# Optimization experiments

Measured on AMD Instinct MI355X. Metric: run time of the kernel, lower is better.

Reference implementation:

```python
import jax, jax.numpy as jnp
import numpy as np

N = 100000
E = 1000000
N_FEAT = 128
N_HID = 16
N_HEAD = 8
HIDDEN = N_HID * N_HEAD  # 128
N_CLASS = 64
NEG_SLOPE = 0.2


def layer_norm(x, g, b, eps=1e-5):
    mu = x.mean(-1, keepdims=True)
    var = ((x - mu) ** 2).mean(-1, keepdims=True)
    return (x - mu) * jax.lax.rsqrt(var + eps) * g + b


def gat_conv(x, src, dst, W, a_src, a_dst, bias, concat):
    # Standard GATConv math (PyG): project, per-head additive attention,
    # softmax over incoming edges (self-loops included), weighted scatter-sum.
    H, C = a_src.shape
    n = x.shape[0]
    h = (x @ W).reshape(n, H, C)                      # [N,H,C]
    al = jnp.einsum('nhc,hc->nh', h, a_src)           # [N,H]
    ar = jnp.einsum('nhc,hc->nh', h, a_dst)
    e = jax.nn.leaky_relu(al[src] + ar[dst], NEG_SLOPE)  # [E',H]
    m = jax.ops.segment_max(e, dst, num_segments=n)
    m = jnp.where(jnp.isfinite(m), m, 0.0)
    ee = jnp.exp(e - m[dst])
    den = jax.ops.segment_sum(ee, dst, num_segments=n)
    alpha = ee / (den[dst] + 1e-16)                   # [E',H]
    out = jax.ops.segment_sum(h[src] * alpha[:, :, None], dst, num_segments=n)
    out = out.reshape(n, H * C) if concat else out.mean(1)
    return out + bias, h, alpha


def setup_inputs() -> dict:
    key = jax.random.key(0)
    ks = jax.random.split(key, 20)
    s = lambda *sh: 1.0 / np.sqrt(sh[-1])
    inp = {
        'x': jax.random.normal(ks[0], (N, N_FEAT), jnp.float32),
        'edge_index': jax.random.randint(ks[1], (2, E), 0, N, jnp.int32),
        # layer 1: n_feat -> n_hid x n_head (concat)
        'W1': jax.random.normal(ks[2], (N_FEAT, HIDDEN), jnp.float32) * s(N_FEAT),
        'a_src1': jax.random.normal(ks[3], (N_HEAD, N_HID), jnp.float32) * s(N_HID),
        'a_dst1': jax.random.normal(ks[4], (N_HEAD, N_HID), jnp.float32) * s(N_HID),
        'b1': jnp.zeros((HIDDEN,), jnp.float32),
        'g1': jnp.ones((HIDDEN,), jnp.float32),
        'be1': jnp.zeros((HIDDEN,), jnp.float32),
        # layer 2: hidden -> hidden (concat)
        'W2': jax.random.normal(ks[5], (HIDDEN, HIDDEN), jnp.float32) * s(HIDDEN),
        'a_src2': jax.random.normal(ks[6], (N_HEAD, N_HID), jnp.float32) * s(N_HID),
        'a_dst2': jax.random.normal(ks[7], (N_HEAD, N_HID), jnp.float32) * s(N_HID),
        'b2': jnp.zeros((HIDDEN,), jnp.float32),
        'g2': jnp.ones((HIDDEN,), jnp.float32),
        'be2': jnp.zeros((HIDDEN,), jnp.float32),
        # out layer: hidden -> n_class, 1 head, concat=False
        'W3': jax.random.normal(ks[8], (HIDDEN, N_CLASS), jnp.float32) * s(HIDDEN),
        'a_src3': jax.random.normal(ks[9], (1, N_CLASS), jnp.float32) * s(N_CLASS),
        'a_dst3': jax.random.normal(ks[10], (1, N_CLASS), jnp.float32) * s(N_CLASS),
        'b3': jnp.zeros((N_CLASS,), jnp.float32),
        'g3': jnp.ones((N_CLASS,), jnp.float32),
        'be3': jnp.zeros((N_CLASS,), jnp.float32),
    }
    return inp


def reference(x, edge_index, W1, a_src1, a_dst1, b1, g1, be1,
              W2, a_src2, a_dst2, b2, g2, be2,
              W3, a_src3, a_dst3, b3, g3, be3):
    # add self loops (GATConv default)
    loops = jnp.arange(N, dtype=edge_index.dtype)
    src = jnp.concatenate([edge_index[0], loops])
    dst = jnp.concatenate([edge_index[1], loops])
    # Transductive path, eval mode (dropout is identity)
    x, _, _ = gat_conv(x, src, dst, W1, a_src1, a_dst1, b1, concat=True)
    x = jax.nn.elu(layer_norm(x, g1, be1))
    x, _, _ = gat_conv(x, src, dst, W2, a_src2, a_dst2, b2, concat=True)
    x = jax.nn.elu(layer_norm(x, g2, be2))
    x, _, _ = gat_conv(x, src, dst, W3, a_src3, a_dst3, b3, concat=False)
    x = layer_norm(x, g3, be3)
    return x
```

## Files before the change

### kernel.cpp

```cpp
#include <hip/hip_runtime.h>
#include <math.h>

#define N_NODES 100000
#define N_EDGES 1000000
#define EP_EDGES (N_EDGES + N_NODES)
#define NBKT ((N_NODES + 255) / 256)
#define PAD 48
#define NB_COUNT ((EP_EDGES + 4095) / 4096)
#define NB_WT ((128 * 128 + 128 * 64 + 255) / 256)

typedef short bf16x8 __attribute__((ext_vector_type(8)));
typedef float f32x4 __attribute__((ext_vector_type(4)));


__device__ inline unsigned bf16pack(float a, float b) {
    unsigned ua = __float_as_uint(a);
    unsigned ub = __float_as_uint(b);
    ua += 0x7FFFu + ((ua >> 16) & 1u);
    ub += 0x7FFFu + ((ub >> 16) & 1u);
    return (ua >> 16) | (ub & 0xFFFF0000u);
}

__device__ inline unsigned short bf16r(float a) {
    unsigned u = __float_as_uint(a);
    u += 0x7FFFu + ((u >> 16) & 1u);
    return (unsigned short)(u >> 16);
}

__device__ inline float bf16f(unsigned short v) {
    return __uint_as_float(((unsigned)v) << 16);
}

__device__ inline int swz(int o) { return o ^ (((o >> 8) & 7) << 4); }


__global__ void prep_count(const int* __restrict__ ei, int* __restrict__ bktCnt,
                           const float* __restrict__ W1, const float* __restrict__ W2,
                           const float* __restrict__ W3, unsigned short* __restrict__ Wt1,
                           unsigned short* __restrict__ Wt2, unsigned short* __restrict__ Wt3) {
    __shared__ int hist[NBKT];
    int tid = threadIdx.x;
    int b = blockIdx.x;
    if (b < NB_COUNT) {
        for (int j = tid; j < NBKT; j += 256) hist[j] = 0;
        __syncthreads();
        int e0 = b * 4096;
        int e1 = min(e0 + 4096, EP_EDGES);
        for (int e = e0 + tid; e < e1; e += 256) {
            int d = (e < N_EDGES) ? ei[N_EDGES + e] : (e - N_EDGES);
            atomicAdd(&hist[d >> 8], 1);
        }
        __syncthreads();
        for (int j = tid; j < NBKT; j += 256) {
            int c = hist[j];
            if (c) atomicAdd(&bktCnt[j], c);
        }
    } else {
        int t = (b - NB_COUNT) * 256 + tid;
        if (t < 128 * 128) {
            int k = t >> 7, c = t & 127;
            Wt1[c * 128 + k] = bf16r(W1[t]);
            Wt2[c * 128 + k] = bf16r(W2[t]);
        }
        int t3 = t - 128 * 128;
        if (t3 >= 0 && t3 < 128 * 64) {
            int k = t3 >> 6, c = t3 & 63;
            Wt3[c * 128 + k] = bf16r(W3[t3]);
        }
    }
}

__global__ void bkt_scan(const int* __restrict__ bktCnt, int* __restrict__ bktBase,
                         int* __restrict__ bktCursor) {
    __shared__ int tmp[512];
    int tid = threadIdx.x;
    int v = (tid < NBKT) ? bktCnt[tid] : 0;
    tmp[tid] = v;
    __syncthreads();
    int run = v;
    for (int off = 1; off < 512; off <<= 1) {
        int add = (tid >= off) ? tmp[tid - off] : 0;
        __syncthreads();
        run += add;
        tmp[tid] = run;
        __syncthreads();
    }
    if (tid <= NBKT) {
        int base = run - v;
        bktBase[tid] = base;
        if (tid < NBKT) bktCursor[tid] = base;
    }
}

__global__ void bkt_scatter(const int* __restrict__ ei, int* __restrict__ bktCursor,
                            unsigned* __restrict__ bktEdges) {
    __shared__ int hist[NBKT], chunk[NBKT];
    int tid = threadIdx.x;
    for (int j = tid; j < NBKT; j += 256) hist[j] = 0;
    __syncthreads();
    int e0 = blockIdx.x * 2048;
    int e1 = min(e0 + 2048, EP_EDGES);
    for (int e = e0 + tid; e < e1; e += 256) {
        int d = (e < N_EDGES) ? ei[N_EDGES + e] : (e - N_EDGES);
        atomicAdd(&hist[d >> 8], 1);
    }
    __syncthreads();
    for (int j = tid; j < NBKT; j += 256) {
        int c = hist[j];
        chunk[j] = c ? atomicAdd(&bktCursor[j], c) : 0;
        hist[j] = 0;
    }
    __syncthreads();
    for (int e = e0 + tid; e < e1; e += 256) {
        int s, d;
        if (e < N_EDGES) { s = ei[e]; d = ei[N_EDGES + e]; }
        else             { s = d = e - N_EDGES; }
        int b = d >> 8;
        int off = atomicAdd(&hist[b], 1);
        bktEdges[chunk[b] + off] = (unsigned)s | ((unsigned)(d & 255) << 24);
    }
}

__global__ void bkt_final(const unsigned* __restrict__ bktEdges, const int* __restrict__ bktBase,
                          int* __restrict__ deg_arr, int* __restrict__ pad_src) {
    __shared__ int hist[256], cur[256];
    int tid = threadIdx.x;
    int b = blockIdx.x;
    int base = bktBase[b], end = bktBase[b + 1];
    hist[tid] = 0;
    cur[tid] = 0;
    __syncthreads();
    for (int i = base + tid; i < end; i += 256)
        atomicAdd(&hist[bktEdges[i] >> 24], 1);
    __syncthreads();
    int node = b * 256 + tid;
    if (node < N_NODES) deg_arr[node] = min(hist[tid], PAD);
    __syncthreads();
    for (int i = base + tid; i < end; i += 256) {
        unsigned u = bktEdges[i];
        int d = u >> 24;
        int pos = atomicAdd(&cur[d], 1);
        if (pos < PAD)
            pad_src[(size_t)(b * 256 + d) * PAD + pos] = (int)(u & 0xFFFFFFu);
    }
    __syncthreads();
    for (int idx = tid; idx < 256 * PAD; idx += 256) {
        int dloc = idx / PAD, j = idx % PAD;
        int nd = b * 256 + dloc;
        if (nd < N_NODES) {
            int dg = min(hist[dloc], PAD);
            int lim = min(PAD, max(16, dg + 7));
            if (j >= dg && j < lim)
                pad_src[(size_t)nd * PAD + j] = nd;
        }
    }
}


template <int COUT, int H, bool IN_F32>
__launch_bounds__(256)
__global__ void gemm_mfma(const void* __restrict__ Xv, const unsigned short* __restrict__ Wt,
                          const float* __restrict__ a_src, const float* __restrict__ a_dst,
                          unsigned* __restrict__ hb16, unsigned short* __restrict__ alb,
                          float* __restrict__ ar, int n) {
    constexpr int NT = COUT / 16;
    __shared__ unsigned char lds[16384 + COUT * 256 + 1024];
    unsigned char* sx = lds;
    unsigned char* sw = lds + 16384;
    float* sc = (float*)sw;

    int tid = threadIdx.x;
    int row0 = blockIdx.x * 64;
    int lane = tid & 63;
    int wv = tid >> 6;

    if (IN_F32) {
        const float* Xf = (const float*)Xv;
        for (int c = tid; c < 1024; c += 256) {
            int o = c * 16;
            int row = o >> 8;
            int k0 = (o & 255) >> 1;
            int gr = row0 + row;
            float4 f0 = make_float4(0.f, 0.f, 0.f, 0.f), f1 = f0;
            if (gr < n) {
                f0 = *(const float4*)(Xf + (size_t)gr * 128 + k0);
                f1 = *(const float4*)(Xf + (size_t)gr * 128 + k0 + 4);
            }
            *(uint4*)(sx + swz(o)) = make_uint4(bf16pack(f0.x, f0.y), bf16pack(f0.z, f0.w),
                                                bf16pack(f1.x, f1.y), bf16pack(f1.z, f1.w));
        }
    } else {
        const unsigned char* Xb = (const unsigned char*)Xv;
        for (int c = tid; c < 1024; c += 256) {
            int o = c * 16;
            int row = o >> 8;
            int gr = row0 + row;
            uint4 v = make_uint4(0u, 0u, 0u, 0u);
            if (gr < n) v = *(const uint4*)(Xb + (size_t)gr * 256 + (o & 255));
            *(uint4*)(sx + swz(o)) = v;
        }
    }
    for (int c = tid; c < COUT * 16; c += 256) {
        int o = c * 16;
        *(uint4*)(sw + swz(o)) = *(const uint4*)((const unsigned char*)Wt + o);
    }
    __syncthreads();

    f32x4 acc[NT];
#pragma unroll
    for (int t = 0; t < NT; ++t) acc[t] = (f32x4){0.f, 0.f, 0.f, 0.f};
    int arow = wv * 16 + (lane & 15);
    int kg = lane >> 4;
#pragma unroll
    for (int s = 0; s < 4; ++s) {
        int ko = s * 64 + kg * 16;
        bf16x8 a = *(const bf16x8*)(sx + swz(arow * 256 + ko));
#pragma unroll
        for (int t = 0; t < NT; ++t) {
            bf16x8 bfr = *(const bf16x8*)(sw + swz((t * 16 + (lane & 15)) * 256 + ko));
            acc[t] = __builtin_amdgcn_mfma_f32_16x16x32_bf16(a, bfr, acc[t], 0, 0, 0);
        }
    }
    __syncthreads();

#pragma unroll
    for (int t = 0; t < NT; ++t)
#pragma unroll
        for (int i = 0; i < 4; ++i)
            sc[(wv * 16 + kg * 4 + i) * (COUT + 4) + t * 16 + (lane & 15)] = acc[t][i];
    __syncthreads();

    constexpr int NCG = COUT / 8;
    constexpr int ROWS = 64 * NCG / 256;
    int tc = tid % NCG, tr = tid / NCG;
    float asv[8], adv[8];
#pragma unroll
    for (int j = 0; j < 8; ++j) {
        asv[j] = a_src[tc * 8 + j];
        adv[j] = a_dst[tc * 8 + j];
    }
#pragma unroll
    for (int i = 0; i < ROWS; ++i) {
        int row = tr * ROWS + i;
        int gr = row0 + row;
        float h8[8];
        *(float4*)&h8[0] = *(const float4*)(sc + row * (COUT + 4) + tc * 8);
        *(float4*)&h8[4] = *(const float4*)(sc + row * (COUT + 4) + tc * 8 + 4);
        float pa = 0.f, pb = 0.f;
#pragma unroll
        for (int j = 0; j < 8; ++j) {
            pa = fmaf(h8[j], asv[j], pa);
            pb = fmaf(h8[j], adv[j], pb);
        }
        if (COUT / H == 16) {
            pa += __shfl_xor(pa, 1);
            pb += __shfl_xor(pb, 1);
            if ((tc & 1) == 0 && gr < n) {
                alb[gr * H + (tc >> 1)] = bf16r(pa);
                ar[gr * H + (tc >> 1)] = pb;
            }
        } else {
            pa += __shfl_xor(pa, 1); pb += __shfl_xor(pb, 1);
            pa += __shfl_xor(pa, 2); pb += __shfl_xor(pb, 2);
            pa += __shfl_xor(pa, 4); pb += __shfl_xor(pb, 4);
            if (tc == 0 && gr < n) {
                alb[gr] = bf16r(pa);
                ar[gr] = pb;
            }
        }
        if (gr < n) {
            *(uint4*)(hb16 + (size_t)gr * (COUT / 2) + tc * 4) =
                make_uint4(bf16pack(h8[0], h8[1]), bf16pack(h8[2], h8[3]),
                           bf16pack(h8[4], h8[5]), bf16pack(h8[6], h8[7]));
        }
    }
}


__launch_bounds__(1024)
__global__ void gat128_k(const unsigned* __restrict__ hb16, const unsigned short* __restrict__ alb,
                         const float* __restrict__ ar, const int* __restrict__ deg_arr,
                         const int* __restrict__ pad_src, const float* __restrict__ bias,
                         const float* __restrict__ gamma, const float* __restrict__ beta,
                         unsigned* __restrict__ outx, int n) {
    __shared__ float wbuf[16][128];
    int tid = threadIdx.x;
    int l = tid & 63;
    int wv = tid >> 6;
    int node = blockIdx.x * 16 + wv;
    node = __builtin_amdgcn_readfirstlane(node);
    if (node >= n) return;

    int deg = deg_arr[node];
    const int* sp = pad_src + (size_t)node * PAD;
    const unsigned char* hbB = (const unsigned char*)hb16;
    const unsigned char* albB = (const unsigned char*)alb;

    unsigned loff = (unsigned)l * 4u;
    int eh = l & 7;
    int ej = l >> 3;
    int hc = l >> 3;
    int c0 = 2 * l;
    float ar_e = ar[node * 8 + eh];
    bool hi = deg > 8;

    float acc0 = 0.f, acc1 = 0.f;

    int s_lo = sp[ej];
    float a_lo = bf16f(*(const unsigned short*)(albB + (((unsigned)s_lo) << 4) + ((unsigned)eh << 1)));
    unsigned rv_lo[8];
#pragma unroll
    for (int j = 0; j < 8; ++j) {
        int sj = __builtin_amdgcn_readlane(s_lo, j * 8);
        rv_lo[j] = *(const unsigned*)(hbB + (((unsigned)sj) << 8) + loff);
    }
    float e0 = a_lo + ar_e; e0 = (e0 >= 0.f) ? e0 : 0.2f * e0;
    float w_lo = (ej < deg) ? __expf(e0) : 0.f;
    float w_hi = 0.f;
    unsigned rv_hi[8];
    if (hi) {
        int s_hi = sp[8 + ej];
        float a_hi = bf16f(*(const unsigned short*)(albB + (((unsigned)s_hi) << 4) + ((unsigned)eh << 1)));
#pragma unroll
        for (int j = 0; j < 8; ++j) {
            int sj = __builtin_amdgcn_readlane(s_hi, j * 8);
            rv_hi[j] = *(const unsigned*)(hbB + (((unsigned)sj) << 8) + loff);
        }
        float e1 = a_hi + ar_e; e1 = (e1 >= 0.f) ? e1 : 0.2f * e1;
        w_hi = (8 + ej < deg) ? __expf(e1) : 0.f;
    }
    float den_bf = w_lo + w_hi;

    *(float2*)&wbuf[wv][2 * l] = make_float2(w_lo, w_hi);
#pragma unroll
    for (int j = 0; j < 8; ++j) {
        float2 wj = *(const float2*)&wbuf[wv][2 * (j * 8 + hc)];
        acc0 = fmaf(wj.x, __uint_as_float(rv_lo[j] << 16), acc0);
        acc1 = fmaf(wj.x, __uint_as_float(rv_lo[j]), acc1);
        if (hi) {
            acc0 = fmaf(wj.y, __uint_as_float(rv_hi[j] << 16), acc0);
            acc1 = fmaf(wj.y, __uint_as_float(rv_hi[j]), acc1);
        }
    }

    for (int k = 16; k < deg; k += 8) {
        int s_c = sp[k + ej];
        float a = bf16f(*(const unsigned short*)(albB + (((unsigned)s_c) << 4) + ((unsigned)eh << 1)));
        float e = a + ar_e; e = (e >= 0.f) ? e : 0.2f * e;
        float w = (k + ej < deg) ? __expf(e) : 0.f;
        den_bf += w;
        unsigned rv[8];
#pragma unroll
        for (int j = 0; j < 8; ++j) {
            int sj = __builtin_amdgcn_readlane(s_c, j * 8);
            rv[j] = *(const unsigned*)(hbB + (((unsigned)sj) << 8) + loff);
        }
#pragma unroll
        for (int j = 0; j < 8; ++j) {
            float wj = __shfl(w, j * 8 + hc);
            acc0 = fmaf(wj, __uint_as_float(rv[j] << 16), acc0);
            acc1 = fmaf(wj, __uint_as_float(rv[j]), acc1);
        }
    }

    den_bf += __shfl_xor(den_bf, 8);
    den_bf += __shfl_xor(den_bf, 16);
    den_bf += __shfl_xor(den_bf, 32);
    float den = __shfl(den_bf, hc);

    float2 bb = *(const float2*)(bias + c0);
    float2 gg = *(const float2*)(gamma + c0);
    float2 tt = *(const float2*)(beta + c0);
    float inv = 1.f / (den + 1e-16f);
    float v0 = acc0 * inv + bb.x;
    float v1 = acc1 * inv + bb.y;
    float ssum = v0 + v1;
    for (int off = 1; off < 64; off <<= 1) ssum += __shfl_xor(ssum, off);
    float mean = ssum * (1.f / 128.f);
    float d0 = v0 - mean, d1 = v1 - mean;
    float vs = d0 * d0 + d1 * d1;
    for (int off = 1; off < 64; off <<= 1) vs += __shfl_xor(vs, off);
    float rstd = rsqrtf(vs * (1.f / 128.f) + 1e-5f);
    float y0 = d0 * rstd * gg.x + tt.x;
    y0 = (y0 > 0.f) ? y0 : (__expf(y0) - 1.f);
    float y1 = d1 * rstd * gg.y + tt.y;
    y1 = (y1 > 0.f) ? y1 : (__expf(y1) - 1.f);
    outx[(size_t)node * 64 + l] = bf16pack(y0, y1);
}


__launch_bounds__(1024)
__global__ void gat64_k(const unsigned* __restrict__ hb16, const unsigned short* __restrict__ alb,
                        const float* __restrict__ ar, const int* __restrict__ deg_arr,
                        const int* __restrict__ pad_src, const float* __restrict__ bias,
                        const float* __restrict__ gamma, const float* __restrict__ beta,
                        float* __restrict__ outx, int n) {
    int tid = threadIdx.x;
    int l = tid & 63;
    int wv = tid >> 6;
    int node = blockIdx.x * 16 + wv;
    node = __builtin_amdgcn_readfirstlane(node);
    if (node >= n) return;

    int deg = deg_arr[node];
    const int* sp = pad_src + (size_t)node * PAD;
    const unsigned char* hbB = (const unsigned char*)hb16;
    const unsigned char* albB = (const unsigned char*)alb;
    unsigned loff2 = (unsigned)l * 2u;

    float ar_e = ar[node];
    int slot = (l < deg) ? l : 0;
    int s_cur = sp[slot];
    float a = bf16f(*(const unsigned short*)(albB + ((unsigned)s_cur << 1)));
    float e = a + ar_e; e = (e >= 0.f) ? e : 0.2f * e;
    float w = (l < deg) ? __expf(e) : 0.f;
    float den = w;
    den += __shfl_xor(den, 1);
    den += __shfl_xor(den, 2);
    den += __shfl_xor(den, 4);
    den += __shfl_xor(den, 8);
    den += __shfl_xor(den, 16);
    den += __shfl_xor(den, 32);

    float acc0 = 0.f;
    int nsub = (deg + 7) >> 3;
    for (int sub = 0; sub < nsub; ++sub) {
#pragma unroll
        for (int j2 = 0; j2 < 8; ++j2) {
            int lidx = sub * 8 + j2;
            int sj = __builtin_amdgcn_readlane(s_cur, lidx);
            float wj = __uint_as_float(__builtin_amdgcn_readlane(__float_as_uint(w), lidx));
            unsigned short rvs = *(const unsigned short*)(hbB + (((unsigned)sj) << 7) + loff2);
            acc0 = fmaf(wj, __uint_as_float(((unsigned)rvs) << 16), acc0);
        }
    }

    float b0 = bias[l], g0 = gamma[l], t0 = beta[l];
    float inv = 1.f / (den + 1e-16f);
    float v0 = acc0 * inv + b0;
    float ssum = v0;
    for (int off = 1; off < 64; off <<= 1) ssum += __shfl_xor(ssum, off);
    float mean = ssum * (1.f / 64.f);
    float d0 = v0 - mean;
    float vs = d0 * d0;
    for (int off = 1; off < 64; off <<= 1) vs += __shfl_xor(vs, off);
    float rstd = rsqrtf(vs * (1.f / 64.f) + 1e-5f);
    outx[(size_t)node * 64 + l] = d0 * rstd * g0 + t0;
}


extern "C" void kernel_launch(void* const* d_in, const int* in_sizes, int n_in,
                              void* d_out, int out_size, void* d_ws, size_t ws_size,
                              hipStream_t stream) {
    const float* x   = (const float*)d_in[0];
    const int*   ei  = (const int*)d_in[1];
    const float* W1  = (const float*)d_in[2];
    const float* as1 = (const float*)d_in[3];
    const float* ad1 = (const float*)d_in[4];
    const float* b1  = (const float*)d_in[5];
    const float* g1  = (const float*)d_in[6];
    const float* be1 = (const float*)d_in[7];
    const float* W2  = (const float*)d_in[8];
    const float* as2 = (const float*)d_in[9];
    const float* ad2 = (const float*)d_in[10];
    const float* b2  = (const float*)d_in[11];
    const float* g2  = (const float*)d_in[12];
    const float* be2 = (const float*)d_in[13];
    const float* W3  = (const float*)d_in[14];
    const float* as3 = (const float*)d_in[15];
    const float* ad3 = (const float*)d_in[16];
    const float* b3  = (const float*)d_in[17];
    const float* g3  = (const float*)d_in[18];
    const float* be3 = (const float*)d_in[19];
    float* out = (float*)d_out;

    char* p = (char*)d_ws;
    auto alloc = [&](size_t bytes) -> char* {
        char* r = p;
        p += (bytes + 255) & ~size_t(255);
        return r;
    };
    unsigned* hb16   = (unsigned*)alloc((size_t)N_NODES * 64 * 4);
    unsigned* xbuf   = (unsigned*)alloc((size_t)N_NODES * 64 * 4);
    unsigned short* alb = (unsigned short*)alloc((size_t)N_NODES * 8 * 2);
    float* ar        = (float*)alloc((size_t)N_NODES * 8 * 4);
    int*   deg_arr   = (int*)alloc((size_t)N_NODES * 4);
    int*   pad_src   = (int*)alloc((size_t)N_NODES * PAD * 4);
    unsigned* bktEdges = (unsigned*)alloc((size_t)EP_EDGES * 4);
    int*   bktCnt    = (int*)alloc((size_t)(NBKT + 1) * 4);
    int*   bktBase   = (int*)alloc((size_t)(NBKT + 1) * 4);
    int*   bktCursor = (int*)alloc((size_t)(NBKT + 1) * 4);
    unsigned short* Wt1 = (unsigned short*)alloc((size_t)128 * 128 * 2);
    unsigned short* Wt2 = (unsigned short*)alloc((size_t)128 * 128 * 2);
    unsigned short* Wt3 = (unsigned short*)alloc((size_t)64 * 128 * 2);

    hipMemsetAsync(bktCnt, 0, (size_t)(NBKT + 1) * 4, stream);

    prep_count<<<NB_COUNT + NB_WT, 256, 0, stream>>>(ei, bktCnt, W1, W2, W3, Wt1, Wt2, Wt3);
    bkt_scan<<<1, 512, 0, stream>>>(bktCnt, bktBase, bktCursor);
    bkt_scatter<<<(EP_EDGES + 2047) / 2048, 256, 0, stream>>>(ei, bktCursor, bktEdges);
    bkt_final<<<NBKT, 256, 0, stream>>>(bktEdges, bktBase, deg_arr, pad_src);

    const int gemm_grid = (N_NODES + 63) / 64;
    const int agg_grid  = (N_NODES + 15) / 16;

    gemm_mfma<128, 8, true><<<gemm_grid, 256, 0, stream>>>(x, Wt1, as1, ad1,
                                                           hb16, alb, ar, N_NODES);
    gat128_k<<<agg_grid, 1024, 0, stream>>>(hb16, alb, ar, deg_arr, pad_src,
                                            b1, g1, be1, xbuf, N_NODES);
    gemm_mfma<128, 8, false><<<gemm_grid, 256, 0, stream>>>(xbuf, Wt2, as2, ad2,
                                                            hb16, alb, ar, N_NODES);
    gat128_k<<<agg_grid, 1024, 0, stream>>>(hb16, alb, ar, deg_arr, pad_src,
                                            b2, g2, be2, xbuf, N_NODES);
    gemm_mfma<64, 1, false><<<gemm_grid, 256, 0, stream>>>(xbuf, Wt3, as3, ad3,
                                                           hb16, alb, ar, N_NODES);
    gat64_k<<<agg_grid, 1024, 0, stream>>>(hb16, alb, ar, deg_arr, pad_src,
                                           b3, g3, be3, out, N_NODES);
}
```

Measured before the change: 280.9 us.

## Fuse edge bucket scatter with layer-1 GEMM and shrink aggregation blocks

Merges the bucket-scatter kernel and the first-layer MFMA projection into one launch, using disjoint block ranges, so the independent scatter and GEMM work can run concurrently and one launch is saved. The GEMM body becomes a device function that the fused kernel shares. Separately, the aggregation kernels drop from 1024-thread blocks (16 nodes) to 256-thread blocks (4 nodes), which may improve scheduling granularity and tail behaviour. The fused kernel's LDS size is set by the GEMM, which may limit occupancy for the scatter blocks.

```diff
diff --git a/kernel.cpp b/kernel.cpp
--- a/kernel.cpp
+++ b/kernel.cpp
@@ -8,6 +8,8 @@
 #define PAD 48
 #define NB_COUNT ((EP_EDGES + 4095) / 4096)
 #define NB_WT ((128 * 128 + 128 * 64 + 255) / 256)
+#define NB_SCAT ((EP_EDGES + 2047) / 2048)
+#define GEMM_GRID ((N_NODES + 63) / 64)
 
 typedef short bf16x8 __attribute__((ext_vector_type(8)));
 typedef float f32x4 __attribute__((ext_vector_type(4)));
@@ -92,85 +94,23 @@
     }
 }
 
-__global__ void bkt_scatter(const int* __restrict__ ei, int* __restrict__ bktCursor,
-                            unsigned* __restrict__ bktEdges) {
-    __shared__ int hist[NBKT], chunk[NBKT];
-    int tid = threadIdx.x;
-    for (int j = tid; j < NBKT; j += 256) hist[j] = 0;
-    __syncthreads();
-    int e0 = blockIdx.x * 2048;
-    int e1 = min(e0 + 2048, EP_EDGES);
-    for (int e = e0 + tid; e < e1; e += 256) {
-        int d = (e < N_EDGES) ? ei[N_EDGES + e] : (e - N_EDGES);
-        atomicAdd(&hist[d >> 8], 1);
-    }
-    __syncthreads();
-    for (int j = tid; j < NBKT; j += 256) {
-        int c = hist[j];
-        chunk[j] = c ? atomicAdd(&bktCursor[j], c) : 0;
-        hist[j] = 0;
-    }
-    __syncthreads();
-    for (int e = e0 + tid; e < e1; e += 256) {
-        int s, d;
-        if (e < N_EDGES) { s = ei[e]; d = ei[N_EDGES + e]; }
-        else             { s = d = e - N_EDGES; }
-        int b = d >> 8;
-        int off = atomicAdd(&hist[b], 1);
-        bktEdges[chunk[b] + off] = (unsigned)s | ((unsigned)(d & 255) << 24);
-    }
-}
-
-__global__ void bkt_final(const unsigned* __restrict__ bktEdges, const int* __restrict__ bktBase,
-                          int* __restrict__ deg_arr, int* __restrict__ pad_src) {
-    __shared__ int hist[256], cur[256];
-    int tid = threadIdx.x;
-    int b = blockIdx.x;
-    int base = bktBase[b], end = bktBase[b + 1];
-    hist[tid] = 0;
-    cur[tid] = 0;
-    __syncthreads();
-    for (int i = base + tid; i < end; i += 256)
-        atomicAdd(&hist[bktEdges[i] >> 24], 1);
-    __syncthreads();
-    int node = b * 256 + tid;
-    if (node < N_NODES) deg_arr[node] = min(hist[tid], PAD);
-    __syncthreads();
-    for (int i = base + tid; i < end; i += 256) {
-        unsigned u = bktEdges[i];
-        int d = u >> 24;
-        int pos = atomicAdd(&cur[d], 1);
-        if (pos < PAD)
-            pad_src[(size_t)(b * 256 + d) * PAD + pos] = (int)(u & 0xFFFFFFu);
-    }
-    __syncthreads();
-    for (int idx = tid; idx < 256 * PAD; idx += 256) {
-        int dloc = idx / PAD, j = idx % PAD;
-        int nd = b * 256 + dloc;
-        if (nd < N_NODES) {
-            int dg = min(hist[dloc], PAD);
-            int lim = min(PAD, max(16, dg + 7));
-            if (j >= dg && j < lim)
-                pad_src[(size_t)nd * PAD + j] = nd;
-        }
-    }
-}
-
 
 template <int COUT, int H, bool IN_F32>
-__launch_bounds__(256)
-__global__ void gemm_mfma(const void* __restrict__ Xv, const unsigned short* __restrict__ Wt,
-                          const float* __restrict__ a_src, const float* __restrict__ a_dst,
-                          unsigned* __restrict__ hb16, unsigned short* __restrict__ alb,
-                          float* __restrict__ ar, int n) {
+__device__ __forceinline__ void gemm_body(unsigned char* lds, int bid,
+                                          const void* __restrict__ Xv,
+                                          const unsigned short* __restrict__ Wt,
+                                          const float* __restrict__ a_src,
+                                          const float* __restrict__ a_dst,
+                                          unsigned* __restrict__ hb16,
+                                          unsigned short* __restrict__ alb,
+                                          float* __restrict__ ar, int n) {
     constexpr int NT = COUT / 16;
-    __shared__ unsigned char lds[16384 + COUT * 256 + 1024];
     unsigned char* sx = lds;
     unsigned char* sw = lds + 16384;
     float* sc = (float*)sw;
 
     int tid = threadIdx.x;
-    int row0 = blockIdx.x * 64;
+    int row0 = bid * 64;
     int lane = tid & 63;
     int wv = tid >> 6;
 
@@ -276,18 +216,105 @@
     }
 }
 
-
-__launch_bounds__(1024)
+template <int COUT, int H, bool IN_F32>
+__launch_bounds__(256)
+__global__ void gemm_mfma(const void* __restrict__ Xv, const unsigned short* __restrict__ Wt,
+                          const float* __restrict__ a_src, const float* __restrict__ a_dst,
+                          unsigned* __restrict__ hb16, unsigned short* __restrict__ alb,
+                          float* __restrict__ ar, int n) {
+    __shared__ unsigned char lds[16384 + COUT * 256 + 1024];
+    gemm_body<COUT, H, IN_F32>(lds, blockIdx.x, Xv, Wt, a_src, a_dst, hb16, alb, ar, n);
+}
+
+
+__launch_bounds__(256)
+__global__ void scat_gemm1(const int* __restrict__ ei, int* __restrict__ bktCursor,
+                           unsigned* __restrict__ bktEdges,
+                           const float* __restrict__ x, const unsigned short* __restrict__ Wt1,
+                           const float* __restrict__ as1, const float* __restrict__ ad1,
+                           unsigned* __restrict__ hb16, unsigned short* __restrict__ alb,
+                           float* __restrict__ ar, int n) {
+    __shared__ unsigned char lds[16384 + 128 * 256 + 1024];
+    int b = blockIdx.x;
+    int tid = threadIdx.x;
+    if (b < NB_SCAT) {
+        int* hist = (int*)lds;
+        int* chunk = hist + NBKT;
+        for (int j = tid; j < NBKT; j += 256) hist[j] = 0;
+        __syncthreads();
+        int e0 = b * 2048;
+        int e1 = min(e0 + 2048, EP_EDGES);
+        for (int e = e0 + tid; e < e1; e += 256) {
+            int d = (e < N_EDGES) ? ei[N_EDGES + e] : (e - N_EDGES);
+            atomicAdd(&hist[d >> 8], 1);
+        }
+        __syncthreads();
+        for (int j = tid; j < NBKT; j += 256) {
+            int c = hist[j];
+            chunk[j] = c ? atomicAdd(&bktCursor[j], c) : 0;
+            hist[j] = 0;
+        }
+        __syncthreads();
+        for (int e = e0 + tid; e < e1; e += 256) {
+            int s, d;
+            if (e < N_EDGES) { s = ei[e]; d = ei[N_EDGES + e]; }
+            else             { s = d = e - N_EDGES; }
+            int bk = d >> 8;
+            int off = atomicAdd(&hist[bk], 1);
+            bktEdges[chunk[bk] + off] = (unsigned)s | ((unsigned)(d & 255) << 24);
+        }
+    } else {
+        gemm_body<128, 8, true>(lds, b - NB_SCAT, x, Wt1, as1, ad1, hb16, alb, ar, n);
+    }
+}
+
+__global__ void bkt_final(const unsigned* __restrict__ bktEdges, const int* __restrict__ bktBase,
+                          int* __restrict__ deg_arr, int* __restrict__ pad_src) {
+    __shared__ int hist[256], cur[256];
+    int tid = threadIdx.x;
+    int b = blockIdx.x;
+    int base = bktBase[b], end = bktBase[b + 1];
+    hist[tid] = 0;
+    cur[tid] = 0;
+    __syncthreads();
+    for (int i = base + tid; i < end; i += 256)
+        atomicAdd(&hist[bktEdges[i] >> 24], 1);
+    __syncthreads();
+    int node = b * 256 + tid;
+    if (node < N_NODES) deg_arr[node] = min(hist[tid], PAD);
+    __syncthreads();
+    for (int i = base + tid; i < end; i += 256) {
+        unsigned u = bktEdges[i];
+        int d = u >> 24;
+        int pos = atomicAdd(&cur[d], 1);
+        if (pos < PAD)
+            pad_src[(size_t)(b * 256 + d) * PAD + pos] = (int)(u & 0xFFFFFFu);
+    }
+    __syncthreads();
+    for (int idx = tid; idx < 256 * PAD; idx += 256) {
+        int dloc = idx / PAD, j = idx % PAD;
+        int nd = b * 256 + dloc;
+        if (nd < N_NODES) {
+            int dg = min(hist[dloc], PAD);
+            int lim = min(PAD, max(16, dg + 7));
+            if (j >= dg && j < lim)
+                pad_src[(size_t)nd * PAD + j] = nd;
+        }
+    }
+}
+
+
+__launch_bounds__(256)
 __global__ void gat128_k(const unsigned* __restrict__ hb16, const unsigned short* __restrict__ alb,
                          const float* __restrict__ ar, const int* __restrict__ deg_arr,
                          const int* __restrict__ pad_src, const float* __restrict__ bias,
                          const float* __restrict__ gamma, const float* __restrict__ beta,
                          unsigned* __restrict__ outx, int n) {
-    __shared__ float wbuf[16][128];
+    __shared__ float wbuf[4][128];
     int tid = threadIdx.x;
     int l = tid & 63;
     int wv = tid >> 6;
-    int node = blockIdx.x * 16 + wv;
+    int node = blockIdx.x * 4 + wv;
     node = __builtin_amdgcn_readfirstlane(node);
     if (node >= n) return;
 
@@ -389,7 +416,7 @@
 }
 
 
-__launch_bounds__(1024)
+__launch_bounds__(256)
 __global__ void gat64_k(const unsigned* __restrict__ hb16, const unsigned short* __restrict__ alb,
                         const float* __restrict__ ar, const int* __restrict__ deg_arr,
                         const int* __restrict__ pad_src, const float* __restrict__ bias,
@@ -398,7 +425,7 @@
     int tid = threadIdx.x;
     int l = tid & 63;
     int wv = tid >> 6;
-    int node = blockIdx.x * 16 + wv;
+    int node = blockIdx.x * 4 + wv;
     node = __builtin_amdgcn_readfirstlane(node);
     if (node >= n) return;
 
@@ -498,22 +525,21 @@
 
     prep_count<<<NB_COUNT + NB_WT, 256, 0, stream>>>(ei, bktCnt, W1, W2, W3, Wt1, Wt2, Wt3);
     bkt_scan<<<1, 512, 0, stream>>>(bktCnt, bktBase, bktCursor);
-    bkt_scatter<<<(EP_EDGES + 2047) / 2048, 256, 0, stream>>>(ei, bktCursor, bktEdges);
+    scat_gemm1<<<NB_SCAT + GEMM_GRID, 256, 0, stream>>>(ei, bktCursor, bktEdges,
+                                                        x, Wt1, as1, ad1,
+                                                        hb16, alb, ar, N_NODES);
     bkt_final<<<NBKT, 256, 0, stream>>>(bktEdges, bktBase, deg_arr, pad_src);
 
-    const int gemm_grid = (N_NODES + 63) / 64;
-    const int agg_grid  = (N_NODES + 15) / 16;
-
-    gemm_mfma<128, 8, true><<<gemm_grid, 256, 0, stream>>>(x, Wt1, as1, ad1,
+    const int agg_grid = (N_NODES + 3) / 4;
+
+    gat128_k<<<agg_grid, 256, 0, stream>>>(hb16, alb, ar, deg_arr, pad_src,
+                                           b1, g1, be1, xbuf, N_NODES);
+    gemm_mfma<128, 8, false><<<GEMM_GRID, 256, 0, stream>>>(xbuf, Wt2, as2, ad2,
+                                                            hb16, alb, ar, N_NODES);
+    gat128_k<<<agg_grid, 256, 0, stream>>>(hb16, alb, ar, deg_arr, pad_src,
+                                           b2, g2, be2, xbuf, N_NODES);
+    gemm_mfma<64, 1, false><<<GEMM_GRID, 256, 0, stream>>>(xbuf, Wt3, as3, ad3,
                                                            hb16, alb, ar, N_NODES);
-    gat128_k<<<agg_grid, 1024, 0, stream>>>(hb16, alb, ar, deg_arr, pad_src,
-                                            b1, g1, be1, xbuf, N_NODES);
-    gemm_mfma<128, 8, false><<<gemm_grid, 256, 0, stream>>>(xbuf, Wt2, as2, ad2,
-                                                            hb16, alb, ar, N_NODES);
-    gat128_k<<<agg_grid, 1024, 0, stream>>>(hb16, alb, ar, deg_arr, pad_src,
-                                            b2, g2, be2, xbuf, N_NODES);
-    gemm_mfma<64, 1, false><<<gemm_grid, 256, 0, stream>>>(xbuf, Wt3, as3, ad3,
-                                                           hb16, alb, ar, N_NODES);
-    gat64_k<<<agg_grid, 1024, 0, stream>>>(hb16, alb, ar, deg_arr, pad_src,
-                                           b3, g3, be3, out, N_NODES);
-}
+    gat64_k<<<agg_grid, 256, 0, stream>>>(hb16, alb, ar, deg_arr, pad_src,
+                                          b3, g3, be3, out, N_NODES);
+}
```

After: 253.1 us. 1.11x faster.
